# Kernel optimization log

Hardware: AMD Instinct MI355X
Metric: run time of the kernel (lower is better)

The kernel has to match this reference:

```python
import jax, jax.numpy as jnp
import numpy as np

N0, N1, N2, N3 = 200000, 50000, 12000, 3000
E0, E1, E2 = 500000, 120000, 30000
D_IN, D_H, D_OUT = 256, 256, 64


def setup_inputs() -> dict:
    key = jax.random.key(0)
    ks = jax.random.split(key, 16)
    s = 1.0 / np.sqrt(D_IN)
    return {
        "x": jax.random.normal(ks[0], (N0, D_IN), jnp.float32),
        "src0": jax.random.randint(ks[1], (E0,), 0, N0),
        "dst0": jax.random.randint(ks[2], (E0,), 0, N1),
        "src1": jax.random.randint(ks[3], (E1,), 0, N1),
        "dst1": jax.random.randint(ks[4], (E1,), 0, N2),
        "src2": jax.random.randint(ks[5], (E2,), 0, N2),
        "dst2": jax.random.randint(ks[6], (E2,), 0, N3),
        "num_dst0": N1, "num_dst1": N2, "num_dst2": N3,
        "Ws0": jax.random.normal(ks[7], (D_IN, D_H), jnp.float32) * s,
        "Wn0": jax.random.normal(ks[8], (D_IN, D_H), jnp.float32) * s,
        "b0": jnp.zeros((D_H,), jnp.float32),
        "Ws1": jax.random.normal(ks[9], (D_H, D_H), jnp.float32) * s,
        "Wn1": jax.random.normal(ks[10], (D_H, D_H), jnp.float32) * s,
        "b1": jnp.zeros((D_H,), jnp.float32),
        "Ws2": jax.random.normal(ks[11], (D_H, D_OUT), jnp.float32) * s,
        "Wn2": jax.random.normal(ks[12], (D_H, D_OUT), jnp.float32) * s,
        "b2": jnp.zeros((D_OUT,), jnp.float32),
    }


def sage_conv(src, dst, num_dst, h_src, Wn, Ws, b):
    # DGL SAGEConv(mean): fc_self(h_dst) + fc_neigh(mean_{in-edges} h_src) + bias
    h_dst = h_src[:num_dst]
    msg = h_src[src]                                          # [E, d] gather
    agg = jax.ops.segment_sum(msg, dst, num_segments=num_dst)  # [num_dst, d]
    deg = jax.ops.segment_sum(jnp.ones((dst.shape[0],), h_src.dtype), dst,
                              num_segments=num_dst)
    h_neigh = agg / jnp.maximum(deg, 1.0)[:, None]
    return h_dst @ Ws + h_neigh @ Wn + b


def reference(x, src0, dst0, src1, dst1, src2, dst2,
              num_dst0, num_dst1, num_dst2,
              Ws0, Wn0, b0, Ws1, Wn1, b1, Ws2, Wn2, b2):
    h = sage_conv(src0, dst0, num_dst0, x, Wn0, Ws0, b0)       # layer 0 (no act, per source)
    h = sage_conv(src1, dst1, num_dst1, h, Wn1, Ws1, b1)       # layer 1
    h = jax.nn.relu(h)                                         # activation after middle layer
    # dropout omitted (eval / deterministic mode)
    h = sage_conv(src2, dst2, num_dst2, h, Wn2, Ws2, b2)       # layer 2
    return h
```

## Files before the change

kernel.cpp:

```cpp
#include <hip/hip_runtime.h>

#define N0_SRC 200000
#define N1_DST 50000
#define N2_DST 12000
#define N3_DST 3000
#define NTOT_DST 65000
#define DH 256
#define DOUT 64
#define EMAX_TOT 650000

typedef __attribute__((ext_vector_type(8))) short short8;
typedef __attribute__((ext_vector_type(4))) float f32x4;

__device__ __forceinline__ ushort f2bf(float f) {
    union { float f; uint32_t u; } v; v.f = f;
    uint32_t r = (v.u + 0x7FFF + ((v.u >> 16) & 1)) >> 16;
    return (ushort)r;
}
__device__ __forceinline__ float bf2f(ushort u) {
    union { uint32_t u; float f; } v; v.u = ((uint32_t)u) << 16;
    return v.f;
}

__device__ __forceinline__ void gload16(const ushort* g, ushort* l) {
    __builtin_amdgcn_global_load_lds(
        (const __attribute__((address_space(1))) unsigned int*)g,
        (__attribute__((address_space(3))) unsigned int*)l,
        16, 0, 0);
}

__global__ void f32_to_bf16_kernel(const float* __restrict__ in,
                                   ushort* __restrict__ out, long n) {
    long i = ((long)blockIdx.x * 256 + threadIdx.x) * 4;
    if (i >= n) return;
    float4 v = *(const float4*)(in + i);
    ushort4 o;
    o.x = f2bf(v.x); o.y = f2bf(v.y); o.z = f2bf(v.z); o.w = f2bf(v.w);
    *(ushort4*)(out + i) = o;
}

__global__ void transpose_w_all(const float* __restrict__ W0, const float* __restrict__ W1,
                                const float* __restrict__ W2, const float* __restrict__ W3,
                                const float* __restrict__ W4, const float* __restrict__ W5,
                                ushort* __restrict__ out, int* __restrict__ cnt) {
    if (blockIdx.y == 0) {
        int z = blockIdx.x * 256 + threadIdx.x;
        if (z < NTOT_DST) cnt[z] = 0;
    }
    const float* W; int Ndim; ushort* o;
    switch (blockIdx.y) {
        case 0: W = W0; Ndim = 256; o = out; break;
        case 1: W = W1; Ndim = 256; o = out + 65536; break;
        case 2: W = W2; Ndim = 256; o = out + 131072; break;
        case 3: W = W3; Ndim = 256; o = out + 196608; break;
        case 4: W = W4; Ndim = 64;  o = out + 262144; break;
        default: W = W5; Ndim = 64; o = out + 278528; break;
    }
    int id = blockIdx.x * 256 + threadIdx.x;
    int n = id >> 8;
    int k = id & 255;
    if (n >= Ndim) return;
    o[id] = f2bf(W[k * Ndim + n]);
}

__global__ void hist3_kernel(const int* __restrict__ d0, int E0,
                             const int* __restrict__ d1, int E1,
                             const int* __restrict__ d2, int E2,
                             int* __restrict__ cnt) {
    int layer = blockIdx.y;
    const int* dst; int E; int base;
    if (layer == 0)      { dst = d0; E = E0; base = 0; }
    else if (layer == 1) { dst = d1; E = E1; base = N1_DST; }
    else                 { dst = d2; E = E2; base = N1_DST + N2_DST; }
    int e = blockIdx.x * 256 + threadIdx.x;
    if (e < E) atomicAdd(&cnt[base + dst[e]], 1);
}

__global__ void fill3_kernel(const int* __restrict__ s0, const int* __restrict__ d0, int E0,
                             const int* __restrict__ s1, const int* __restrict__ d1, int E1,
                             const int* __restrict__ s2, const int* __restrict__ d2, int E2,
                             int* __restrict__ cursor, int* __restrict__ eidx) {
    int layer = blockIdx.y;
    const int* src; const int* dst; int E; int base;
    if (layer == 0)      { src = s0; dst = d0; E = E0; base = 0; }
    else if (layer == 1) { src = s1; dst = d1; E = E1; base = N1_DST; }
    else                 { src = s2; dst = d2; E = E2; base = N1_DST + N2_DST; }
    int e = blockIdx.x * 256 + threadIdx.x;
    if (e < E) {
        int p = atomicAdd(&cursor[base + dst[e]], 1);
        eidx[p] = src[e];
    }
}

__global__ void scan_phase_a(const int* __restrict__ cnt, int* __restrict__ partial, int n) {
    __shared__ int red[4];
    int t = threadIdx.x;
    int i = blockIdx.x * 1024 + t * 4;
    int s = 0;
    if (i + 3 < n) {
        int4 v = *(const int4*)(cnt + i);
        s = v.x + v.y + v.z + v.w;
    }
#pragma unroll
    for (int d = 32; d; d >>= 1) s += __shfl_down(s, d, 64);
    if ((t & 63) == 0) red[t >> 6] = s;
    __syncthreads();
    if (t == 0) partial[blockIdx.x] = red[0] + red[1] + red[2] + red[3];
}

__global__ void scan_phase_b(int* __restrict__ partial, int nb) {
    int t = threadIdx.x;
    int own = (t < nb) ? partial[t] : 0;
    int v = own;
#pragma unroll
    for (int d = 1; d < 64; d <<= 1) {
        int u = __shfl_up(v, d, 64);
        if (t >= d) v += u;
    }
    if (t < nb) partial[t] = v - own;
}

__global__ void scan_phase_c(const int* __restrict__ cnt, const int* __restrict__ partial,
                             int* __restrict__ off, int* __restrict__ cursor, int n) {
    __shared__ int tsum[256];
    int t = threadIdx.x;
    int i = blockIdx.x * 1024 + t * 4;
    int4 c = make_int4(0, 0, 0, 0);
    if (i + 3 < n) c = *(const int4*)(cnt + i);
    int s = c.x + c.y + c.z + c.w;
    tsum[t] = s;
    __syncthreads();
#pragma unroll
    for (int d = 1; d < 256; d <<= 1) {
        int u = (t >= d) ? tsum[t - d] : 0;
        __syncthreads();
        tsum[t] += u;
        __syncthreads();
    }
    int base = partial[blockIdx.x] + tsum[t] - s;
    if (i + 3 < n) {
        int4 ov;
        ov.x = base;
        ov.y = ov.x + c.x;
        ov.z = ov.y + c.y;
        ov.w = ov.z + c.z;
        *(int4*)(off + i) = ov;
        *(int4*)(cursor + i) = ov;
        if (i + 4 == n) off[n] = ov.w + c.w;
    }
}

__global__ void gather_mean_bf16_kernel(const ushort* __restrict__ h,
                                        const int* __restrict__ off,
                                        const int* __restrict__ eidx,
                                        ushort* __restrict__ hn,
                                        int num_dst) {
    int w = blockIdx.x * 4 + (threadIdx.x >> 6);
    int lane = threadIdx.x & 63;
    if (w >= num_dst) return;
    int beg = off[w];
    int end = off[w + 1];
    float a0 = 0.f, a1 = 0.f, a2 = 0.f, a3 = 0.f;
    for (int i = beg; i < end; i += 4) {
        int rem = end - i;
        int j1 = i + (rem > 1 ? 1 : 0);
        int j2 = i + (rem > 2 ? 2 : 0);
        int j3 = i + (rem > 3 ? 3 : 0);
        float m1 = rem > 1 ? 1.f : 0.f;
        float m2 = rem > 2 ? 1.f : 0.f;
        float m3 = rem > 3 ? 1.f : 0.f;
        int s0 = eidx[i], s1 = eidx[j1], s2 = eidx[j2], s3 = eidx[j3];
        ushort4 v0 = ((const ushort4*)(h + (size_t)s0 * DH))[lane];
        ushort4 v1 = ((const ushort4*)(h + (size_t)s1 * DH))[lane];
        ushort4 v2 = ((const ushort4*)(h + (size_t)s2 * DH))[lane];
        ushort4 v3 = ((const ushort4*)(h + (size_t)s3 * DH))[lane];
        a0 += bf2f(v0.x) + m1 * bf2f(v1.x) + m2 * bf2f(v2.x) + m3 * bf2f(v3.x);
        a1 += bf2f(v0.y) + m1 * bf2f(v1.y) + m2 * bf2f(v2.y) + m3 * bf2f(v3.y);
        a2 += bf2f(v0.z) + m1 * bf2f(v1.z) + m2 * bf2f(v2.z) + m3 * bf2f(v3.z);
        a3 += bf2f(v0.w) + m1 * bf2f(v1.w) + m2 * bf2f(v2.w) + m3 * bf2f(v3.w);
    }
    float inv = 1.0f / fmaxf((float)(end - beg), 1.0f);
    ushort4 o;
    o.x = f2bf(a0 * inv); o.y = f2bf(a1 * inv);
    o.z = f2bf(a2 * inv); o.w = f2bf(a3 * inv);
    *(ushort4*)(hn + (size_t)w * DH + lane * 4) = o;
}

template <int MT, int NT, bool RELU, bool OUT_BF16>
__global__ __launch_bounds__(256) void gemm_dual(const ushort* __restrict__ Ad,
                                                 const ushort* __restrict__ An,
                                                 const ushort* __restrict__ Wst,
                                                 const ushort* __restrict__ Wnt,
                                                 const float* __restrict__ bias,
                                                 void* __restrict__ Cv,
                                                 int M, int N) {
    const int K = 256;
    const int BM = MT * 64;
    const int BN = NT * 16;
    __shared__ __align__(16) ushort lds[(2 * BM + 2 * BN) * 32];
    ushort* Asd = lds;
    ushort* Asn = lds + BM * 32;
    ushort* Bss = lds + 2 * BM * 32;
    ushort* Bsn = lds + 2 * BM * 32 + BN * 32;

    int tid  = threadIdx.x;
    int lane = tid & 63;
    int wid  = tid >> 6;
    int q    = lane >> 4;
    int mr   = lane & 15;
    int row0 = blockIdx.y * BM;
    int col0 = blockIdx.x * BN;

    f32x4 acc[MT][NT];
#pragma unroll
    for (int i = 0; i < MT; ++i)
#pragma unroll
        for (int j = 0; j < NT; ++j) acc[i][j] = (f32x4){0.f, 0.f, 0.f, 0.f};

    for (int k0 = 0; k0 < K; k0 += 32) {
#pragma unroll
        for (int c = 0; c < MT; ++c) {
            int chunk = c * 256 + tid;
            int r   = chunk >> 2;
            int sg  = (chunk & 3) ^ ((r >> 1) & 3);
            int row = row0 + r;
            if (row > M - 1) row = M - 1;
            const ushort* gd = Ad + (size_t)row * K + k0 + sg * 8;
            const ushort* gn = An + (size_t)row * K + k0 + sg * 8;
            int cb = (c * 256 + (tid & ~63)) * 8;
            gload16(gd, Asd + cb);
            gload16(gn, Asn + cb);
        }
#pragma unroll
        for (int c = 0; c < NT / 4; ++c) {
            int chunk = c * 256 + tid;
            int r  = chunk >> 2;
            int sg = (chunk & 3) ^ ((r >> 1) & 3);
            const ushort* gs = Wst + (size_t)(col0 + r) * K + k0 + sg * 8;
            const ushort* gw = Wnt + (size_t)(col0 + r) * K + k0 + sg * 8;
            int cb = (c * 256 + (tid & ~63)) * 8;
            gload16(gs, Bss + cb);
            gload16(gw, Bsn + cb);
        }
        __syncthreads();

        short8 ad[MT], an[MT];
#pragma unroll
        for (int mt = 0; mt < MT; ++mt) {
            int rho = wid * (MT * 16) + mt * 16 + mr;
            int o   = rho * 32 + ((q ^ ((rho >> 1) & 3)) * 8);
            ad[mt] = *(const short8*)(Asd + o);
            an[mt] = *(const short8*)(Asn + o);
        }
#pragma unroll
        for (int nt = 0; nt < NT; ++nt) {
            int rho = nt * 16 + mr;
            int o   = rho * 32 + ((q ^ ((rho >> 1) & 3)) * 8);
            short8 bs = *(const short8*)(Bss + o);
            short8 bn = *(const short8*)(Bsn + o);
#pragma unroll
            for (int mt = 0; mt < MT; ++mt) {
                acc[mt][nt] = __builtin_amdgcn_mfma_f32_16x16x32_bf16(
                    ad[mt], bs, acc[mt][nt], 0, 0, 0);
                acc[mt][nt] = __builtin_amdgcn_mfma_f32_16x16x32_bf16(
                    an[mt], bn, acc[mt][nt], 0, 0, 0);
            }
        }
        __syncthreads();
    }

#pragma unroll
    for (int mt = 0; mt < MT; ++mt) {
#pragma unroll
        for (int i = 0; i < 4; ++i) {
            int row = row0 + wid * (MT * 16) + mt * 16 + q * 4 + i;
            if (row >= M) continue;
#pragma unroll
            for (int nt = 0; nt < NT; ++nt) {
                int col = col0 + nt * 16 + mr;
                float v = acc[mt][nt][i] + bias[col];
                if (RELU) v = fmaxf(v, 0.0f);
                if (OUT_BF16) ((ushort*)Cv)[(size_t)row * N + col] = f2bf(v);
                else          ((float*)Cv)[(size_t)row * N + col] = v;
            }
        }
    }
}

extern "C" void kernel_launch(void* const* d_in, const int* in_sizes, int n_in,
                              void* d_out, int out_size, void* d_ws, size_t ws_size,
                              hipStream_t stream) {
    const float* x    = (const float*)d_in[0];
    const int* src0   = (const int*)d_in[1];
    const int* dst0   = (const int*)d_in[2];
    const int* src1   = (const int*)d_in[3];
    const int* dst1   = (const int*)d_in[4];
    const int* src2   = (const int*)d_in[5];
    const int* dst2   = (const int*)d_in[6];
    const float* Ws0  = (const float*)d_in[10];
    const float* Wn0  = (const float*)d_in[11];
    const float* b0   = (const float*)d_in[12];
    const float* Ws1  = (const float*)d_in[13];
    const float* Wn1  = (const float*)d_in[14];
    const float* b1   = (const float*)d_in[15];
    const float* Ws2  = (const float*)d_in[16];
    const float* Wn2  = (const float*)d_in[17];
    const float* b2   = (const float*)d_in[18];
    float* out = (float*)d_out;

    int E0 = in_sizes[1];
    int E1 = in_sizes[3];
    int E2 = in_sizes[5];

    ushort* wsu  = (ushort*)d_ws;
    ushort* xb   = wsu;
    ushort* hn0b = xb   + (size_t)N0_SRC * DH;
    ushort* h1b  = hn0b + (size_t)N1_DST * DH;
    ushort* hn1b = h1b  + (size_t)N1_DST * DH;
    ushort* h2b  = hn1b + (size_t)N2_DST * DH;
    ushort* hn2b = h2b  + (size_t)N2_DST * DH;
    ushort* Wt   = hn2b + (size_t)N3_DST * DH;
    ushort* Ws0t = Wt;
    ushort* Wn0t = Wt + 65536;
    ushort* Ws1t = Wt + 131072;
    ushort* Wn1t = Wt + 196608;
    ushort* Ws2t = Wt + 262144;
    ushort* Wn2t = Wt + 278528;
    int* cnt     = (int*)(Wt + 294912);
    int* off     = cnt + NTOT_DST;
    int* cursor  = off + NTOT_DST + 4;
    int* eidx    = cursor + NTOT_DST;
    int* partial = eidx + EMAX_TOT;

    long nxb = (long)N0_SRC * DH;
    f32_to_bf16_kernel<<<(int)((nxb / 4 + 255) / 256), 256, 0, stream>>>(x, xb, nxb);
    transpose_w_all<<<dim3(256, 6), 256, 0, stream>>>(Ws0, Wn0, Ws1, Wn1, Ws2, Wn2, Wt, cnt);

    int Emax = max(max(E0, E1), E2);
    int nb = (NTOT_DST + 1023) / 1024;
    hist3_kernel<<<dim3((Emax + 255) / 256, 3), 256, 0, stream>>>(dst0, E0, dst1, E1, dst2, E2, cnt);
    scan_phase_a<<<nb, 256, 0, stream>>>(cnt, partial, NTOT_DST);
    scan_phase_b<<<1, 64, 0, stream>>>(partial, nb);
    scan_phase_c<<<nb, 256, 0, stream>>>(cnt, partial, off, cursor, NTOT_DST);
    fill3_kernel<<<dim3((Emax + 255) / 256, 3), 256, 0, stream>>>(
        src0, dst0, E0, src1, dst1, E1, src2, dst2, E2, cursor, eidx);

    const int* off0 = off;
    const int* off1 = off + N1_DST;
    const int* off2 = off + N1_DST + N2_DST;

    gather_mean_bf16_kernel<<<(N1_DST + 3) / 4, 256, 0, stream>>>(xb, off0, eidx, hn0b, N1_DST);
    gemm_dual<2, 8, false, true><<<dim3(DH / 128, (N1_DST + 127) / 128), 256, 0, stream>>>(
        xb, hn0b, Ws0t, Wn0t, b0, h1b, N1_DST, DH);

    gather_mean_bf16_kernel<<<(N2_DST + 3) / 4, 256, 0, stream>>>(h1b, off1, eidx, hn1b, N2_DST);
    gemm_dual<2, 8, true, true><<<dim3(DH / 128, (N2_DST + 127) / 128), 256, 0, stream>>>(
        h1b, hn1b, Ws1t, Wn1t, b1, h2b, N2_DST, DH);

    gather_mean_bf16_kernel<<<(N3_DST + 3) / 4, 256, 0, stream>>>(h2b, off2, eidx, hn2b, N3_DST);
    gemm_dual<1, 4, false, false><<<dim3(DOUT / 64, (N3_DST + 63) / 64), 256, 0, stream>>>(
        h2b, hn2b, Ws2t, Wn2t, b2, out, N3_DST, DOUT);
}
```

Before: 505.7 us.

## Fuse conversion, weight transpose and histogram; fold scan phase; widen gather unroll

```diff
diff --git a/kernel.cpp b/kernel.cpp
--- a/kernel.cpp
+++ b/kernel.cpp
@@ -9,6 +9,9 @@
 #define DOUT 64
 #define EMAX_TOT 650000
 
+#define HIST_BLOCKS 1024
+#define CONV_BLOCKS 3072
+
 typedef __attribute__((ext_vector_type(8))) short short8;
 typedef __attribute__((ext_vector_type(4))) float f32x4;
 
@@ -29,51 +32,48 @@
         16, 0, 0);
 }
 
-__global__ void f32_to_bf16_kernel(const float* __restrict__ in,
-                                   ushort* __restrict__ out, long n) {
-    long i = ((long)blockIdx.x * 256 + threadIdx.x) * 4;
-    if (i >= n) return;
-    float4 v = *(const float4*)(in + i);
-    ushort4 o;
-    o.x = f2bf(v.x); o.y = f2bf(v.y); o.z = f2bf(v.z); o.w = f2bf(v.w);
-    *(ushort4*)(out + i) = o;
-}
-
-__global__ void transpose_w_all(const float* __restrict__ W0, const float* __restrict__ W1,
-                                const float* __restrict__ W2, const float* __restrict__ W3,
-                                const float* __restrict__ W4, const float* __restrict__ W5,
-                                ushort* __restrict__ out, int* __restrict__ cnt) {
-    if (blockIdx.y == 0) {
-        int z = blockIdx.x * 256 + threadIdx.x;
-        if (z < NTOT_DST) cnt[z] = 0;
-    }
-    const float* W; int Ndim; ushort* o;
-    switch (blockIdx.y) {
-        case 0: W = W0; Ndim = 256; o = out; break;
-        case 1: W = W1; Ndim = 256; o = out + 65536; break;
-        case 2: W = W2; Ndim = 256; o = out + 131072; break;
-        case 3: W = W3; Ndim = 256; o = out + 196608; break;
-        case 4: W = W4; Ndim = 64;  o = out + 262144; break;
-        default: W = W5; Ndim = 64; o = out + 278528; break;
-    }
-    int id = blockIdx.x * 256 + threadIdx.x;
-    int n = id >> 8;
-    int k = id & 255;
-    if (n >= Ndim) return;
-    o[id] = f2bf(W[k * Ndim + n]);
-}
-
-__global__ void hist3_kernel(const int* __restrict__ d0, int E0,
-                             const int* __restrict__ d1, int E1,
-                             const int* __restrict__ d2, int E2,
-                             int* __restrict__ cnt) {
-    int layer = blockIdx.y;
-    const int* dst; int E; int base;
-    if (layer == 0)      { dst = d0; E = E0; base = 0; }
-    else if (layer == 1) { dst = d1; E = E1; base = N1_DST; }
-    else                 { dst = d2; E = E2; base = N1_DST + N2_DST; }
-    int e = blockIdx.x * 256 + threadIdx.x;
-    if (e < E) atomicAdd(&cnt[base + dst[e]], 1);
+__global__ __launch_bounds__(256) void conv_trans_hist(
+    const float* __restrict__ x, ushort* __restrict__ xb,
+    const float* __restrict__ W0, const float* __restrict__ W1,
+    const float* __restrict__ W2, const float* __restrict__ W3,
+    const float* __restrict__ W4, const float* __restrict__ W5,
+    ushort* __restrict__ Wt,
+    const int* __restrict__ d0, int E0,
+    const int* __restrict__ d1, int E1,
+    const int* __restrict__ d2, int E2,
+    int* __restrict__ cnt) {
+    int bid = blockIdx.x, t = threadIdx.x;
+    if (bid < HIST_BLOCKS) {
+        const int S = HIST_BLOCKS * 256;
+        int g = bid * 256 + t;
+        for (int e = g; e < E0; e += S) atomicAdd(&cnt[d0[e]], 1);
+        for (int e = g; e < E1; e += S) atomicAdd(&cnt[N1_DST + d1[e]], 1);
+        for (int e = g; e < E2; e += S) atomicAdd(&cnt[N1_DST + N2_DST + d2[e]], 1);
+        return;
+    }
+    const int S = CONV_BLOCKS * 256;
+    int g = (bid - HIST_BLOCKS) * 256 + t;
+    {
+        const float4* xv = (const float4*)x;
+        ushort4* xo = (ushort4*)xb;
+        const int nv = N0_SRC * (DH / 4);
+        for (int i = g; i < nv; i += S) {
+            float4 v = xv[i];
+            ushort4 o;
+            o.x = f2bf(v.x); o.y = f2bf(v.y); o.z = f2bf(v.z); o.w = f2bf(v.w);
+            xo[i] = o;
+        }
+    }
+    for (int i = g; i < 294912; i += S) {
+        const float* W; ushort* o; int id; int Ndim;
+        if (i < 262144) { int wy = i >> 16; id = i & 65535;
+            const float* ws[4] = {W0, W1, W2, W3};
+            W = ws[wy]; o = Wt + (wy << 16); Ndim = 256; }
+        else { int j = i - 262144; int wy = j >> 14; id = j & 16383;
+            W = wy ? W5 : W4; o = Wt + 262144 + (wy << 14); Ndim = 64; }
+        int n = id >> 8, k = id & 255;
+        o[id] = f2bf(W[k * Ndim + n]);
+    }
 }
 
 __global__ void fill3_kernel(const int* __restrict__ s0, const int* __restrict__ d0, int E0,
@@ -108,22 +108,21 @@
     if (t == 0) partial[blockIdx.x] = red[0] + red[1] + red[2] + red[3];
 }
 
-__global__ void scan_phase_b(int* __restrict__ partial, int nb) {
-    int t = threadIdx.x;
-    int own = (t < nb) ? partial[t] : 0;
-    int v = own;
-#pragma unroll
-    for (int d = 1; d < 64; d <<= 1) {
-        int u = __shfl_up(v, d, 64);
-        if (t >= d) v += u;
-    }
-    if (t < nb) partial[t] = v - own;
-}
-
 __global__ void scan_phase_c(const int* __restrict__ cnt, const int* __restrict__ partial,
                              int* __restrict__ off, int* __restrict__ cursor, int n) {
     __shared__ int tsum[256];
+    __shared__ int pbase;
     int t = threadIdx.x;
+    if (t < 64) {
+        int own = partial[t];
+        int v = own;
+#pragma unroll
+        for (int d = 1; d < 64; d <<= 1) {
+            int u = __shfl_up(v, d, 64);
+            if (t >= d) v += u;
+        }
+        if (t == (int)blockIdx.x) pbase = v - own;
+    }
     int i = blockIdx.x * 1024 + t * 4;
     int4 c = make_int4(0, 0, 0, 0);
     if (i + 3 < n) c = *(const int4*)(cnt + i);
@@ -137,7 +136,7 @@
         tsum[t] += u;
         __syncthreads();
     }
-    int base = partial[blockIdx.x] + tsum[t] - s;
+    int base = pbase + tsum[t] - s;
     if (i + 3 < n) {
         int4 ov;
         ov.x = base;
@@ -161,23 +160,40 @@
     int beg = off[w];
     int end = off[w + 1];
     float a0 = 0.f, a1 = 0.f, a2 = 0.f, a3 = 0.f;
-    for (int i = beg; i < end; i += 4) {
+    for (int i = beg; i < end; i += 8) {
         int rem = end - i;
         int j1 = i + (rem > 1 ? 1 : 0);
         int j2 = i + (rem > 2 ? 2 : 0);
         int j3 = i + (rem > 3 ? 3 : 0);
+        int j4 = i + (rem > 4 ? 4 : 0);
+        int j5 = i + (rem > 5 ? 5 : 0);
+        int j6 = i + (rem > 6 ? 6 : 0);
+        int j7 = i + (rem > 7 ? 7 : 0);
         float m1 = rem > 1 ? 1.f : 0.f;
         float m2 = rem > 2 ? 1.f : 0.f;
         float m3 = rem > 3 ? 1.f : 0.f;
-        int s0 = eidx[i], s1 = eidx[j1], s2 = eidx[j2], s3 = eidx[j3];
+        float m4 = rem > 4 ? 1.f : 0.f;
+        float m5 = rem > 5 ? 1.f : 0.f;
+        float m6 = rem > 6 ? 1.f : 0.f;
+        float m7 = rem > 7 ? 1.f : 0.f;
+        int s0 = eidx[i],  s1 = eidx[j1], s2 = eidx[j2], s3 = eidx[j3];
+        int s4 = eidx[j4], s5 = eidx[j5], s6 = eidx[j6], s7 = eidx[j7];
         ushort4 v0 = ((const ushort4*)(h + (size_t)s0 * DH))[lane];
         ushort4 v1 = ((const ushort4*)(h + (size_t)s1 * DH))[lane];
         ushort4 v2 = ((const ushort4*)(h + (size_t)s2 * DH))[lane];
         ushort4 v3 = ((const ushort4*)(h + (size_t)s3 * DH))[lane];
-        a0 += bf2f(v0.x) + m1 * bf2f(v1.x) + m2 * bf2f(v2.x) + m3 * bf2f(v3.x);
-        a1 += bf2f(v0.y) + m1 * bf2f(v1.y) + m2 * bf2f(v2.y) + m3 * bf2f(v3.y);
-        a2 += bf2f(v0.z) + m1 * bf2f(v1.z) + m2 * bf2f(v2.z) + m3 * bf2f(v3.z);
-        a3 += bf2f(v0.w) + m1 * bf2f(v1.w) + m2 * bf2f(v2.w) + m3 * bf2f(v3.w);
+        ushort4 v4 = ((const ushort4*)(h + (size_t)s4 * DH))[lane];
+        ushort4 v5 = ((const ushort4*)(h + (size_t)s5 * DH))[lane];
+        ushort4 v6 = ((const ushort4*)(h + (size_t)s6 * DH))[lane];
+        ushort4 v7 = ((const ushort4*)(h + (size_t)s7 * DH))[lane];
+        a0 += (bf2f(v0.x) + m1 * bf2f(v1.x) + m2 * bf2f(v2.x) + m3 * bf2f(v3.x)) +
+              (m4 * bf2f(v4.x) + m5 * bf2f(v5.x) + m6 * bf2f(v6.x) + m7 * bf2f(v7.x));
+        a1 += (bf2f(v0.y) + m1 * bf2f(v1.y) + m2 * bf2f(v2.y) + m3 * bf2f(v3.y)) +
+              (m4 * bf2f(v4.y) + m5 * bf2f(v5.y) + m6 * bf2f(v6.y) + m7 * bf2f(v7.y));
+        a2 += (bf2f(v0.z) + m1 * bf2f(v1.z) + m2 * bf2f(v2.z) + m3 * bf2f(v3.z)) +
+              (m4 * bf2f(v4.z) + m5 * bf2f(v5.z) + m6 * bf2f(v6.z) + m7 * bf2f(v7.z));
+        a3 += (bf2f(v0.w) + m1 * bf2f(v1.w) + m2 * bf2f(v2.w) + m3 * bf2f(v3.w)) +
+              (m4 * bf2f(v4.w) + m5 * bf2f(v5.w) + m6 * bf2f(v6.w) + m7 * bf2f(v7.w));
     }
     float inv = 1.0f / fmaxf((float)(end - beg), 1.0f);
     ushort4 o;
@@ -259,12 +275,13 @@
             short8 bs = *(const short8*)(Bss + o);
             short8 bn = *(const short8*)(Bsn + o);
 #pragma unroll
-            for (int mt = 0; mt < MT; ++mt) {
+            for (int mt = 0; mt < MT; ++mt)
                 acc[mt][nt] = __builtin_amdgcn_mfma_f32_16x16x32_bf16(
                     ad[mt], bs, acc[mt][nt], 0, 0, 0);
+#pragma unroll
+            for (int mt = 0; mt < MT; ++mt)
                 acc[mt][nt] = __builtin_amdgcn_mfma_f32_16x16x32_bf16(
                     an[mt], bn, acc[mt][nt], 0, 0, 0);
-            }
         }
         __syncthreads();
     }
@@ -332,15 +349,14 @@
     int* eidx    = cursor + NTOT_DST;
     int* partial = eidx + EMAX_TOT;
 
-    long nxb = (long)N0_SRC * DH;
-    f32_to_bf16_kernel<<<(int)((nxb / 4 + 255) / 256), 256, 0, stream>>>(x, xb, nxb);
-    transpose_w_all<<<dim3(256, 6), 256, 0, stream>>>(Ws0, Wn0, Ws1, Wn1, Ws2, Wn2, Wt, cnt);
-
     int Emax = max(max(E0, E1), E2);
     int nb = (NTOT_DST + 1023) / 1024;
-    hist3_kernel<<<dim3((Emax + 255) / 256, 3), 256, 0, stream>>>(dst0, E0, dst1, E1, dst2, E2, cnt);
+
+    hipMemsetAsync(cnt, 0, NTOT_DST * sizeof(int), stream);
+    conv_trans_hist<<<HIST_BLOCKS + CONV_BLOCKS, 256, 0, stream>>>(
+        x, xb, Ws0, Wn0, Ws1, Wn1, Ws2, Wn2, Wt,
+        dst0, E0, dst1, E1, dst2, E2, cnt);
     scan_phase_a<<<nb, 256, 0, stream>>>(cnt, partial, NTOT_DST);
-    scan_phase_b<<<1, 64, 0, stream>>>(partial, nb);
     scan_phase_c<<<nb, 256, 0, stream>>>(cnt, partial, off, cursor, NTOT_DST);
     fill3_kernel<<<dim3((Emax + 255) / 256, 3), 256, 0, stream>>>(
         src0, dst0, E0, src1, dst1, E1, src2, dst2, E2, cursor, eidx);
```

After: 509.0 us. About the same (+0.7%).
